# Kernel optimization log

Measured on AMD Instinct MI355X. Metric: run time of the kernel, lower is better.

Reference implementation:

```python
import jax, jax.numpy as jnp
import numpy as np

IN_SHAPE_DOWN = (8, 16, 8)   # prod = 1024
OUT_SHAPE_DOWN = (4, 4, 4)   # prod = 64
TT_RANK = 8


def tt_to_dense(cores, in_shape, out_shape):
    """Contract TT-matrix cores [r_{k-1}, i_k, j_k, r_k] into a dense (prod_in, prod_out) matrix."""
    res = cores[0]  # [1, i1, j1, r1]
    for c in cores[1:]:
        res = jnp.einsum('...a,aijb->...ijb', res, c)
    res = res[0, ..., 0]  # (i1, j1, i2, j2, ..., id, jd)
    d = len(in_shape)
    perm = [2 * k for k in range(d)] + [2 * k + 1 for k in range(d)]
    return res.transpose(perm).reshape(int(np.prod(in_shape)), int(np.prod(out_shape)))


def setup_inputs() -> dict:
    key = jax.random.key(0)
    ks = jax.random.split(key, 8)
    r = TT_RANK
    # down cores: in factors (8,16,8) -> out factors (4,4,4)
    d1 = 0.1 * jax.random.normal(ks[0], (1, 8, 4, r), dtype=jnp.float32)
    d2 = 0.1 * jax.random.normal(ks[1], (r, 16, 4, r), dtype=jnp.float32)
    d3 = 0.1 * jax.random.normal(ks[2], (r, 8, 4, 1), dtype=jnp.float32)
    # up cores: shape = [reversed(out_down), reversed(in_down)] = [(4,4,4),(8,16,8)]
    u1 = 0.1 * jax.random.normal(ks[3], (1, 4, 8, r), dtype=jnp.float32)
    u2 = 0.1 * jax.random.normal(ks[4], (r, 4, 16, r), dtype=jnp.float32)
    u3 = 0.1 * jax.random.normal(ks[5], (r, 4, 8, 1), dtype=jnp.float32)
    x = jax.random.normal(ks[6], (4, 4096, 1024), dtype=jnp.float32)
    bias_down = 0.001 * jnp.ones((64,), dtype=jnp.float32)
    bias_up = 0.001 * jnp.ones((1024,), dtype=jnp.float32)
    return {"x": x, "d1": d1, "d2": d2, "d3": d3,
            "u1": u1, "u2": u2, "u3": u3,
            "bias_down": bias_down, "bias_up": bias_up}


def reference(x, d1, d2, d3, u1, u2, u3, bias_down, bias_up):
    # Down-project TT matrix: 1024 -> 64
    Wd = tt_to_dense([d1, d2, d3], IN_SHAPE_DOWN, OUT_SHAPE_DOWN)
    # Up-project TT matrix: 64 -> 1024 (reversed factor shapes)
    Wu = tt_to_dense([u1, u2, u3], tuple(reversed(OUT_SHAPE_DOWN)), tuple(reversed(IN_SHAPE_DOWN)))
    z = jnp.einsum('bsd,dk->bsk', x, Wd) + bias_down
    z = jax.nn.relu(z)
    y = jnp.einsum('bsk,kd->bsd', z, Wu) + bias_up
    return y
```

## Files before the change

### kernel.cpp

```cpp
#include <hip/hip_runtime.h>

typedef float f32x2 __attribute__((ext_vector_type(2)));
typedef float f32x4 __attribute__((ext_vector_type(4)));
typedef short short8 __attribute__((ext_vector_type(8)));

static __device__ __forceinline__ unsigned short f2bf(float f) {
    __bf16 h = (__bf16)f;
    return __builtin_bit_cast(unsigned short, h);
}

static __device__ __forceinline__ void gload_lds16(const void* g, void* l) {
    __builtin_amdgcn_global_load_lds(
        (const __attribute__((address_space(1))) void*)g,
        (__attribute__((address_space(3))) void*)l, 16, 0, 0);
}

__global__ __launch_bounds__(256) void tt_build_w_kernel(
    const float* __restrict__ d1, const float* __restrict__ d2, const float* __restrict__ d3,
    const float* __restrict__ u1, const float* __restrict__ u2, const float* __restrict__ u3,
    unsigned short* __restrict__ WdT_sw, unsigned short* __restrict__ WuT_sw)
{
    int t = blockIdx.x * 256 + threadIdx.x;
    if (t < 65536) {
        int j = t >> 10, i = t & 1023;
        int i1 = i >> 7, i2 = (i >> 3) & 15, i3 = i & 7;
        int j1 = j >> 4, j2 = (j >> 2) & 3, j3 = j & 3;
        float t3[8];
#pragma unroll
        for (int b = 0; b < 8; ++b) t3[b] = d3[(b * 8 + i3) * 4 + j3];
        float wsum = 0.f;
#pragma unroll
        for (int a = 0; a < 8; ++a) {
            float va = d1[(i1 * 4 + j1) * 8 + a];
            const float* p2 = d2 + ((a * 16 + i2) * 4 + j2) * 8;
            float wa = 0.f;
#pragma unroll
            for (int b = 0; b < 8; ++b) wa = fmaf(p2[b], t3[b], wa);
            wsum = fmaf(va, wa, wsum);
        }
        int q_ = i >> 8, ck = (i >> 6) & 3, ks2 = (i >> 5) & 1;
        int kg_ = (i >> 3) & 3, m = i & 7;
        int off = (q_ * 4 + ck) * 4096 + ((ks2 * 4 + kg_) * 64 + j) * 8 + m;
        WdT_sw[off] = f2bf(wsum);
    } else {
        int t2 = t - 65536;
        int d = t2 >> 6, k = t2 & 63;
        int k1 = k >> 4, k2 = (k >> 2) & 3, k3 = k & 3;
        int o1 = d >> 7, o2 = (d >> 3) & 15, o3 = d & 7;
        float t3[8];
#pragma unroll
        for (int b = 0; b < 8; ++b) t3[b] = u3[(b * 4 + k3) * 8 + o3];
        float wsum = 0.f;
#pragma unroll
        for (int a = 0; a < 8; ++a) {
            float va = u1[(k1 * 8 + o1) * 8 + a];
            const float* p2 = u2 + ((a * 4 + k2) * 16 + o2) * 8;
            float wa = 0.f;
#pragma unroll
            for (int b = 0; b < 8; ++b) wa = fmaf(p2[b], t3[b], wa);
            wsum = fmaf(va, wa, wsum);
        }
        int dl = d & 511, hf = d >> 9;
        int off = hf * 32768 + (dl * 8 + ((k >> 3) ^ (dl & 7))) * 8 + (k & 7);
        WuT_sw[off] = f2bf(wsum);
    }
}

__global__ __launch_bounds__(256) void tt_fused_kernel(
    const float* __restrict__ x, const unsigned short* __restrict__ WdT_sw,
    const unsigned short* __restrict__ WuT_sw, const float* __restrict__ bd,
    const float* __restrict__ bu, float* __restrict__ y)
{
    __shared__ float red[4][4][1024];
    __shared__ unsigned short zlds[4][16 * 80];
    const int t = threadIdx.x;
    const int lane = t & 63;
    const int h = t >> 6;
    const int l15 = lane & 15;
    const int kg = lane >> 4;
    const int tile0 = blockIdx.x * 4;

    const int colz = (t >> 6) * 16 + (t & 15);
    const int rowz = ((t & 63) >> 4) * 4;
    const float bdv = bd[colz];

    const float* xp0 = x + ((size_t)(tile0 + 0) * 16 + l15) * 1024 + h * 256 + kg * 8;
    const float* xp1 = xp0 + 16 * 1024;
    const float* xp2 = xp0 + 32 * 1024;
    const float* xp3 = xp0 + 48 * 1024;
    const unsigned short* wqb = WdT_sw + h * 16384 + kg * 512 + l15 * 8;
    const unsigned short* wq0 = wqb;
    const unsigned short* wq1 = wqb + 2048;
    const unsigned short* wq2 = wqb + 4096;
    const unsigned short* wq3 = wqb + 6144;
    const unsigned short* wq4 = wqb + 8192;
    const unsigned short* wq5 = wqb + 10240;
    const unsigned short* wq6 = wqb + 12288;
    const unsigned short* wq7 = wqb + 14336;

    f32x4 xA[8], xB[8];
    short8 wA[4], wB[4];
    f32x4 acc[4][4];
#pragma unroll
    for (int t4 = 0; t4 < 4; ++t4)
#pragma unroll
        for (int ct = 0; ct < 4; ++ct) acc[t4][ct] = {0.f, 0.f, 0.f, 0.f};

#define ISSUE(D, W, WQ, O0, O1)                                                                   \
    asm volatile("global_load_dwordx4 %0, %1, off offset:" #O0 : "=v"(D[0]) : "v"(xp0) : "memory"); \
    asm volatile("global_load_dwordx4 %0, %1, off offset:" #O1 : "=v"(D[1]) : "v"(xp0) : "memory"); \
    asm volatile("global_load_dwordx4 %0, %1, off offset:" #O0 : "=v"(D[2]) : "v"(xp1) : "memory"); \
    asm volatile("global_load_dwordx4 %0, %1, off offset:" #O1 : "=v"(D[3]) : "v"(xp1) : "memory"); \
    asm volatile("global_load_dwordx4 %0, %1, off offset:" #O0 : "=v"(D[4]) : "v"(xp2) : "memory"); \
    asm volatile("global_load_dwordx4 %0, %1, off offset:" #O1 : "=v"(D[5]) : "v"(xp2) : "memory"); \
    asm volatile("global_load_dwordx4 %0, %1, off offset:" #O0 : "=v"(D[6]) : "v"(xp3) : "memory"); \
    asm volatile("global_load_dwordx4 %0, %1, off offset:" #O1 : "=v"(D[7]) : "v"(xp3) : "memory"); \
    asm volatile("global_load_dwordx4 %0, %1, off offset:0"   : "=v"(W[0]) : "v"(WQ) : "memory");   \
    asm volatile("global_load_dwordx4 %0, %1, off offset:256" : "=v"(W[1]) : "v"(WQ) : "memory");   \
    asm volatile("global_load_dwordx4 %0, %1, off offset:512" : "=v"(W[2]) : "v"(WQ) : "memory");   \
    asm volatile("global_load_dwordx4 %0, %1, off offset:768" : "=v"(W[3]) : "v"(WQ) : "memory");

#define CPT(D, W, WN) do {                                                                   \
    asm volatile("s_waitcnt vmcnt(" #WN ")" ::: "memory");                                   \
    __builtin_amdgcn_sched_barrier(0);                                                       \
    _Pragma("unroll")                                                                        \
    for (int t4 = 0; t4 < 4; ++t4) {                                                         \
        union { short8 v; unsigned short e[8]; } a;                                          \
        _Pragma("unroll")                                                                    \
        for (int e = 0; e < 4; ++e) {                                                        \
            a.e[e]     = f2bf(D[2 * t4][e]);                                                 \
            a.e[e + 4] = f2bf(D[2 * t4 + 1][e]);                                             \
        }                                                                                    \
        _Pragma("unroll")                                                                    \
        for (int ct = 0; ct < 4; ++ct)                                                       \
            acc[t4][ct] = __builtin_amdgcn_mfma_f32_16x16x32_bf16(a.v, W[ct], acc[t4][ct],   \
                                                                  0, 0, 0);                  \
    }                                                                                        \
    __builtin_amdgcn_sched_barrier(0);                                                       \
} while (0)

    ISSUE(xA, wA, wq0, 0, 16)
    ISSUE(xB, wB, wq1, 128, 144)
    CPT(xA, wA, 12); ISSUE(xA, wA, wq2, 256, 272)
    CPT(xB, wB, 12); ISSUE(xB, wB, wq3, 384, 400)
    CPT(xA, wA, 12); ISSUE(xA, wA, wq4, 512, 528)
    CPT(xB, wB, 12); ISSUE(xB, wB, wq5, 640, 656)
    CPT(xA, wA, 12); ISSUE(xA, wA, wq6, 768, 784)
    CPT(xB, wB, 12); ISSUE(xB, wB, wq7, 896, 912)
    CPT(xA, wA, 12);
    CPT(xB, wB, 0);
#undef ISSUE
#undef CPT

#pragma unroll
    for (int t4 = 0; t4 < 4; ++t4)
#pragma unroll
        for (int ct = 0; ct < 4; ++ct)
            *reinterpret_cast<f32x4*>(&red[t4][h][ct * 256 + lane * 4]) = acc[t4][ct];
    __syncthreads();
#pragma unroll
    for (int t4 = 0; t4 < 4; ++t4) {
        f32x4 v0 = *reinterpret_cast<const f32x4*>(&red[t4][0][t * 4]);
        f32x4 v1 = *reinterpret_cast<const f32x4*>(&red[t4][1][t * 4]);
        f32x4 v2 = *reinterpret_cast<const f32x4*>(&red[t4][2][t * 4]);
        f32x4 v3 = *reinterpret_cast<const f32x4*>(&red[t4][3][t * 4]);
#pragma unroll
        for (int r = 0; r < 4; ++r) {
            float zz = v0[r] + v1[r] + v2[r] + v3[r] + bdv;
            zz = zz > 0.f ? zz : 0.f;
            zlds[t4][(rowz + r) * 80 + colz] = f2bf(zz);
        }
    }
    __syncthreads();

    unsigned short* wlds = reinterpret_cast<unsigned short*>(&red[0][0][0]);
    const int w = h;
#pragma unroll
    for (int ch = 0; ch < 2; ++ch) {
        const unsigned short* src = WuT_sw + ch * 32768 + w * 8192 + lane * 8;
#pragma unroll
        for (int i = 0; i < 16; ++i)
            gload_lds16(src + i * 512, wlds + w * 8192 + i * 512);
        f32x4 bv[8];
#pragma unroll
        for (int i = 0; i < 8; ++i)
            bv[i] = *reinterpret_cast<const f32x4*>(bu + ch * 512 + w * 128 + i * 16 + kg * 4);
        __syncthreads();

#pragma unroll
        for (int tt = 0; tt < 4; ++tt) {
            const int tile = tile0 + tt;
            short8 az0 = *reinterpret_cast<const short8*>(&zlds[tt][l15 * 80 + kg * 8]);
            short8 az1 = *reinterpret_cast<const short8*>(&zlds[tt][l15 * 80 + 32 + kg * 8]);
            const size_t yb = (size_t)(tile * 16 + l15) * 1024 + ch * 512 + w * 128;
#pragma unroll
            for (int i = 0; i < 8; ++i) {
                const int row = w * 128 + i * 16 + l15;
                const int s = row & 7;
                short8 b0 = *reinterpret_cast<const short8*>(&wlds[(row * 8 + (kg ^ s)) * 8]);
                short8 b1 = *reinterpret_cast<const short8*>(&wlds[(row * 8 + ((kg + 4) ^ s)) * 8]);
                f32x4 c = {0.f, 0.f, 0.f, 0.f};
                c = __builtin_amdgcn_mfma_f32_16x16x32_bf16(b0, az0, c, 0, 0, 0);
                c = __builtin_amdgcn_mfma_f32_16x16x32_bf16(b1, az1, c, 0, 0, 0);
                f32x4 o;
#pragma unroll
                for (int r = 0; r < 4; ++r) o[r] = c[r] + bv[i][r];
                *reinterpret_cast<f32x4*>(y + yb + i * 16 + kg * 4) = o;
            }
        }
        __syncthreads();
    }
}

extern "C" void kernel_launch(void* const* d_in, const int* in_sizes, int n_in,
                              void* d_out, int out_size, void* d_ws, size_t ws_size,
                              hipStream_t stream) {
    const float* x  = (const float*)d_in[0];
    const float* d1 = (const float*)d_in[1];
    const float* d2 = (const float*)d_in[2];
    const float* d3 = (const float*)d_in[3];
    const float* u1 = (const float*)d_in[4];
    const float* u2 = (const float*)d_in[5];
    const float* u3 = (const float*)d_in[6];
    const float* bd = (const float*)d_in[7];
    const float* bu = (const float*)d_in[8];
    float* y = (float*)d_out;
    unsigned short* WdT_sw = (unsigned short*)d_ws;
    unsigned short* WuT_sw = WdT_sw + 65536;

    hipLaunchKernelGGL(tt_build_w_kernel, dim3(512), dim3(256), 0, stream,
                       d1, d2, d3, u1, u2, u3, WdT_sw, WuT_sw);
    hipLaunchKernelGGL(tt_fused_kernel, dim3(256), dim3(256), 0, stream,
                       x, WdT_sw, WuT_sw, bd, bu, y);
}
```

Measured before the change: 33.66 us.

## Prefetch first half of up-projection weights into dedicated LDS during down-GEMM tail

Adds a separate 64KB LDS staging buffer for the first half of the up-projection weight matrix and issues its async global-to-LDS loads during the tail of the down-projection MFMA pipeline, so that load latency overlaps compute. The second half is loaded into the reused reduction buffer right after the z computation and is consumed after the first half's GEMM, which removes one barrier round-trip. The cost is extra LDS per block (roughly 64KB more), which may cut occupancy. It also changes the vmcnt wait counts in the final compute steps.

```diff
diff --git a/kernel.cpp b/kernel.cpp
--- a/kernel.cpp
+++ b/kernel.cpp
@@ -72,6 +72,7 @@
     const float* __restrict__ bu, float* __restrict__ y)
 {
     __shared__ float red[4][4][1024];
+    __shared__ unsigned short wstage[32768];
     __shared__ unsigned short zlds[4][16 * 80];
     const int t = threadIdx.x;
     const int lane = t & 63;
@@ -147,8 +148,16 @@
     CPT(xB, wB, 12); ISSUE(xB, wB, wq5, 640, 656)
     CPT(xA, wA, 12); ISSUE(xA, wA, wq6, 768, 784)
     CPT(xB, wB, 12); ISSUE(xB, wB, wq7, 896, 912)
-    CPT(xA, wA, 12);
-    CPT(xB, wB, 0);
+    __builtin_amdgcn_sched_barrier(0);
+    {
+        const unsigned short* src0 = WuT_sw + h * 8192 + lane * 8;
+#pragma unroll
+        for (int i = 0; i < 16; ++i)
+            gload_lds16(src0 + i * 512, wstage + h * 8192 + i * 512);
+    }
+    __builtin_amdgcn_sched_barrier(0);
+    CPT(xA, wA, 28);
+    CPT(xB, wB, 16);
 #undef ISSUE
 #undef CPT
 
@@ -175,24 +184,54 @@
 
     unsigned short* wlds = reinterpret_cast<unsigned short*>(&red[0][0][0]);
     const int w = h;
-#pragma unroll
-    for (int ch = 0; ch < 2; ++ch) {
-        const unsigned short* src = WuT_sw + ch * 32768 + w * 8192 + lane * 8;
+
+    {
+        const unsigned short* src1 = WuT_sw + 32768 + h * 8192 + lane * 8;
 #pragma unroll
         for (int i = 0; i < 16; ++i)
-            gload_lds16(src + i * 512, wlds + w * 8192 + i * 512);
+            gload_lds16(src1 + i * 512, wlds + h * 8192 + i * 512);
+    }
+
+    {
         f32x4 bv[8];
 #pragma unroll
         for (int i = 0; i < 8; ++i)
-            bv[i] = *reinterpret_cast<const f32x4*>(bu + ch * 512 + w * 128 + i * 16 + kg * 4);
-        __syncthreads();
-
+            bv[i] = *reinterpret_cast<const f32x4*>(bu + w * 128 + i * 16 + kg * 4);
 #pragma unroll
         for (int tt = 0; tt < 4; ++tt) {
             const int tile = tile0 + tt;
             short8 az0 = *reinterpret_cast<const short8*>(&zlds[tt][l15 * 80 + kg * 8]);
             short8 az1 = *reinterpret_cast<const short8*>(&zlds[tt][l15 * 80 + 32 + kg * 8]);
-            const size_t yb = (size_t)(tile * 16 + l15) * 1024 + ch * 512 + w * 128;
+            const size_t yb = (size_t)(tile * 16 + l15) * 1024 + w * 128;
+#pragma unroll
+            for (int i = 0; i < 8; ++i) {
+                const int row = w * 128 + i * 16 + l15;
+                const int s = row & 7;
+                short8 b0 = *reinterpret_cast<const short8*>(&wstage[(row * 8 + (kg ^ s)) * 8]);
+                short8 b1 = *reinterpret_cast<const short8*>(&wstage[(row * 8 + ((kg + 4) ^ s)) * 8]);
+                f32x4 c = {0.f, 0.f, 0.f, 0.f};
+                c = __builtin_amdgcn_mfma_f32_16x16x32_bf16(b0, az0, c, 0, 0, 0);
+                c = __builtin_amdgcn_mfma_f32_16x16x32_bf16(b1, az1, c, 0, 0, 0);
+                f32x4 o;
+#pragma unroll
+                for (int r = 0; r < 4; ++r) o[r] = c[r] + bv[i][r];
+                *reinterpret_cast<f32x4*>(y + yb + i * 16 + kg * 4) = o;
+            }
+        }
+    }
+    __syncthreads();
+
+    {
+        f32x4 bv[8];
+#pragma unroll
+        for (int i = 0; i < 8; ++i)
+            bv[i] = *reinterpret_cast<const f32x4*>(bu + 512 + w * 128 + i * 16 + kg * 4);
+#pragma unroll
+        for (int tt = 0; tt < 4; ++tt) {
+            const int tile = tile0 + tt;
+            short8 az0 = *reinterpret_cast<const short8*>(&zlds[tt][l15 * 80 + kg * 8]);
+            short8 az1 = *reinterpret_cast<const short8*>(&zlds[tt][l15 * 80 + 32 + kg * 8]);
+            const size_t yb = (size_t)(tile * 16 + l15) * 1024 + 512 + w * 128;
 #pragma unroll
             for (int i = 0; i < 8; ++i) {
                 const int row = w * 128 + i * 16 + l15;
@@ -208,7 +247,6 @@
                 *reinterpret_cast<f32x4*>(y + yb + i * 16 + kg * 4) = o;
             }
         }
-        __syncthreads();
     }
 }
 
```

Result: no change. 33.34 us (median of 2 runs) (-0.9%).
